# Kernel tuning notes

Hardware: AMD Instinct MI355X
Metric: run time of the kernel (lower is better)

## Reference

```python
import math
from collections import deque
import jax, jax.numpy as jnp
import numpy as np

PS = 16; DF = 256; DS = 16; DLANG = 896; BETA = 2.0
B_SZ = 2; IMG = 512


def setup_inputs():
    key = jax.random.key(0)
    ks = jax.random.split(key, 16)
    def rn(k, shape, scale=1.0):
        return jax.random.normal(k, shape, jnp.float32) * scale
    # W_delta bias init: inverse-softplus of dt ~ LogUniform(1e-3, 1e-1), as in torch _init_weights
    u = jax.random.uniform(ks[15], (DF,), jnp.float32)
    dt = jnp.exp(u * (math.log(0.1) - math.log(0.001)) + math.log(0.001))
    inv_dt = dt + jnp.log(-jnp.expm1(-dt))
    return {
        "images": rn(ks[0], (B_SZ, 3, IMG, IMG)),
        "lang_g": rn(ks[1], (B_SZ, DLANG)),
        "conv1_w": rn(ks[2], (64, 3, 3, 3), 1.0 / math.sqrt(27)),
        "conv1_b": jnp.zeros((64,), jnp.float32),
        "conv2_w": rn(ks[3], (128, 64, 3, 3), 1.0 / math.sqrt(576)),
        "conv2_b": jnp.zeros((128,), jnp.float32),
        "fc_w": rn(ks[4], (DF, 128), 1.0 / math.sqrt(128)),
        "fc_b": jnp.zeros((DF,), jnp.float32),
        "W_gate": rn(ks[5], (DF, DLANG), 1.0 / math.sqrt(DLANG)),
        "W_g_prime": rn(ks[6], (DF, DLANG), 1.0 / math.sqrt(DLANG)),
        "A_log": jnp.log(jnp.broadcast_to(jnp.arange(1, DS + 1, dtype=jnp.float32), (DF, DS))),
        "D": jnp.ones((DF,), jnp.float32),
        "B_w": rn(ks[7], (DS, DF), 1.0 / math.sqrt(DF)),
        "B_b": jnp.zeros((DS,), jnp.float32),
        "C_w": rn(ks[8], (DS, DF), 1.0 / math.sqrt(DF)),
        "C_b": jnp.zeros((DS,), jnp.float32),
        "Wd_w": rn(ks[9], (DF, DF), 1.0 / math.sqrt(DF)),
        "Wd_b": inv_dt,
        "out_w": rn(ks[10], (DF, DF), 1.0 / math.sqrt(DF)),
        "out_b": jnp.zeros((DF,), jnp.float32),
        "ln_g": jnp.ones((DF,), jnp.float32),
        "ln_b": jnp.zeros((DF,), jnp.float32),
    }


def _gelu(x):
    return jax.nn.gelu(x, approximate=False)  # torch nn.GELU() default = exact erf


def _conv(x, w, b):
    y = jax.lax.conv_general_dilated(x, w, (1, 1), 'SAME', dimension_numbers=('NCHW', 'OIHW', 'NCHW'))
    return y + b[None, :, None, None]


def _patch_feats(images, c1w, c1b, c2w, c2b, fcw, fcb):
    B, C, H, W = images.shape
    nH, nW = H // PS, W // PS
    # non-overlapping patchify (== unfold/unfold in torch)
    p = images.reshape(B, C, nH, PS, nW, PS).transpose(0, 2, 4, 1, 3, 5).reshape(B * nH * nW, C, PS, PS)
    h = _gelu(_conv(p, c1w, c1b))
    h = _gelu(_conv(h, c2w, c2b))
    h = h.mean(axis=(2, 3))  # AdaptiveAvgPool2d((1,1))
    feats = (h @ fcw.T + fcb).reshape(B, nH * nW, DF)
    return feats, nH, nW


def _structure(feats, r_sem, nH, nW):
    # Host-side (numpy) Kruskal MST + BFS ordering, mirroring the torch detach().cpu() path.
    f = np.asarray(feats, np.float32)
    r = np.asarray(r_sem, np.float32)
    B, P, _ = f.shape
    src, dst = [], []
    for i in range(nH):
        for j in range(nW):
            u = i * nW + j
            if j + 1 < nW:
                src.append(u); dst.append(u + 1)
            if i + 1 < nH:
                src.append(u); dst.append(u + nW)
    src = np.array(src); dst = np.array(dst)
    bfs_all, par_all = [], []
    for b in range(B):
        fn = f[b] / np.maximum(np.linalg.norm(f[b], axis=1, keepdims=True), 1e-12)
        cos = (fn[src] * fn[dst]).sum(1)
        w = (1.0 - r[b][src]) * (1.0 - r[b][dst]) * (-cos) + 1e-6
        parent = np.arange(P)
        def find(x):
            while parent[x] != x:
                parent[x] = parent[parent[x]]
                x = parent[x]
            return x
        adj = [[] for _ in range(P)]
        cnt = 0
        for idx in np.argsort(w):
            ru, rv = find(int(src[idx])), find(int(dst[idx]))
            if ru != rv:
                parent[ru] = rv
                adj[src[idx]].append(int(dst[idx]))
                adj[dst[idx]].append(int(src[idx]))
                cnt += 1
                if cnt == P - 1:
                    break
        root = int(r[b].argmax())
        vis = [False] * P; par_of = [-1] * P; bfs = []
        q = deque([root]); vis[root] = True
        while q:
            n = q.popleft()
            bfs.append(n)
            for nb in adj[n]:
                if not vis[nb]:
                    vis[nb] = True
                    par_of[nb] = n
                    q.append(nb)
        o2b = [0] * P
        for bi, oi in enumerate(bfs):
            o2b[oi] = bi
        par_bfs = [-1 if par_of[o] == -1 else o2b[par_of[o]] for o in bfs]
        bfs_all.append(bfs); par_all.append(par_bfs)
    return jnp.array(bfs_all, jnp.int32), jnp.array(par_all, jnp.int32)


def _core(feats, r_sem, g_prime, bfs, par, A_log, D, B_w, B_b, C_w, C_b, Wd_w, Wd_b, out_w, out_b, ln_g, ln_b):
    A = -jnp.exp(A_log)  # (DF, DS)
    def one(f_b, r_b, gp, bfs_b, par_b):
        rs = r_b[bfs_b]                                  # (P,)
        X = f_b[bfs_b] + rs[:, None] * gp[None, :]       # (P, DF)
        delta = jax.nn.softplus(X @ Wd_w.T + Wd_b) * (1.0 + BETA * rs[:, None])
        Bp = X @ B_w.T + B_b                             # (P, DS)
        Cp = X @ C_w.T + C_b                             # (P, DS)
        P = X.shape[0]
        def body(H, inp):
            i, d_i, b_i, c_i, x_i, p_i = inp
            A_bar = jnp.exp(d_i[:, None] * A)            # (DF, DS)
            h_par = H[jnp.maximum(p_i, 0)] * (p_i >= 0)  # zeros at root
            h = A_bar * h_par + (d_i[:, None] * b_i[None, :]) * x_i[:, None]
            H = H.at[i].set(h)
            y = (h * c_i[None, :]).sum(-1) + D * x_i
            return H, y
        H0 = jnp.zeros((P, DF, DS), X.dtype)
        _, Y = jax.lax.scan(body, H0, (jnp.arange(P), delta, Bp, Cp, X, par_b))
        Yr = jnp.zeros_like(Y).at[bfs_b].set(Y)          # scatter back to raster order
        o = Yr @ out_w.T + out_b
        mu = o.mean(-1, keepdims=True)
        v = ((o - mu) ** 2).mean(-1, keepdims=True)
        return ln_g * (o - mu) / jnp.sqrt(v + 1e-5) + ln_b
    return jax.vmap(one)(feats, r_sem, g_prime, bfs, par)


def reference(images, lang_g, conv1_w, conv1_b, conv2_w, conv2_b, fc_w, fc_b, W_gate, W_g_prime, A_log, D, B_w, B_b, C_w, C_b, Wd_w, Wd_b, out_w, out_b, ln_g, ln_b):
    feats, nH, nW = _patch_feats(images, conv1_w, conv1_b, conv2_w, conv2_b, fc_w, fc_b)
    g_proj = lang_g @ W_gate.T
    r_sem = jax.nn.sigmoid(jnp.einsum('bd,bpd->bp', g_proj, feats) / math.sqrt(DF))
    bfs, par = _structure(feats, r_sem, nH, nW)
    g_prime = lang_g @ W_g_prime.T
    return _core(feats, r_sem, g_prime, bfs, par, A_log, D, B_w, B_b, C_w, C_b, Wd_w, Wd_b, out_w, out_b, ln_g, ln_b)
```

## Files before the change

kernel.cpp:

```cpp
#include <hip/hip_runtime.h>
#include <cstddef>
#include <cstdint>

#define NB    2
#define NP    1024
#define DFEAT 256
#define DSTATE 16
#define NEDGE 1984

typedef unsigned short ushortb;

typedef float fx16 __attribute__((ext_vector_type(16)));
typedef short s16x8 __attribute__((ext_vector_type(8)));

__device__ __forceinline__ float bf2f(unsigned short u){
  union { unsigned int i; float f; } c; c.i = ((unsigned int)u) << 16; return c.f;
}
__device__ __forceinline__ unsigned short f2bf(float f){
  union { float f; unsigned int i; } c; c.f = f;
  unsigned int u = c.i;
  unsigned int r = (u + 0x7fffu + ((u >> 16) & 1u)) >> 16;
  return (unsigned short)r;
}
__device__ __forceinline__ float ldin(const void* p, size_t i, int isbf){
  return isbf ? bf2f(((const ushortb*)p)[i]) : ((const float*)p)[i];
}
__device__ __forceinline__ float gelu_f(float x){
  return 0.5f * x * (1.0f + erff(x * 0.70710678118654752f));
}
__device__ __forceinline__ unsigned int f2sort(float f){
  union { float f; unsigned int i; } c; c.f = f;
  return (c.i & 0x80000000u) ? ~c.i : (c.i | 0x80000000u);
}

constexpr size_t AL(size_t x){ return (x + 63) & ~(size_t)63; }
constexpr size_t O_W1    = 0;
constexpr size_t O_B1    = AL(O_W1 + 1728);
constexpr size_t O_W2    = AL(O_B1 + 64);
constexpr size_t O_B2    = AL(O_W2 + 73728);
constexpr size_t O_FCW   = AL(O_B2 + 128);
constexpr size_t O_FCB   = AL(O_FCW + 32768);
constexpr size_t O_WDW   = AL(O_FCB + 256);
constexpr size_t O_WDB   = AL(O_WDW + 65536);
constexpr size_t O_BWO   = AL(O_WDB + 256);
constexpr size_t O_BBO   = AL(O_BWO + 4096);
constexpr size_t O_CWO   = AL(O_BBO + 16);
constexpr size_t O_CBO   = AL(O_CWO + 4096);
constexpr size_t O_OW    = AL(O_CBO + 16);
constexpr size_t O_OB    = AL(O_OW + 65536);
constexpr size_t O_AF    = AL(O_OB + 256);
constexpr size_t O_DD    = AL(O_AF + 4096);
constexpr size_t O_LNG   = AL(O_DD + 256);
constexpr size_t O_LNB   = AL(O_LNG + 256);
constexpr size_t O_FEATS = AL(O_LNB + 256);
constexpr size_t O_GPROJ = AL(O_FEATS + (size_t)NB*NP*DFEAT);
constexpr size_t O_GPRIM = AL(O_GPROJ + NB*DFEAT);
constexpr size_t O_RSEM  = AL(O_GPRIM + NB*DFEAT);
constexpr size_t O_BFS   = AL(O_RSEM + NB*NP);
constexpr size_t O_PAR   = AL(O_BFS + NB*NP);
constexpr size_t O_X     = AL(O_PAR + NB*NP);
constexpr size_t O_DELTA = AL(O_X + (size_t)NB*NP*DFEAT);
constexpr size_t O_BP    = AL(O_DELTA + (size_t)NB*NP*DFEAT);
constexpr size_t O_CP    = AL(O_BP + NB*NP*DSTATE);
constexpr size_t O_YR    = AL(O_CP + NB*NP*DSTATE);
constexpr size_t O_FLAG  = AL(O_YR + (size_t)NB*NP*DFEAT);
constexpr size_t O_LVL   = AL(O_FLAG + 64);

__global__ __launch_bounds__(256) void k_sniff(const void* img, float* ws)
{
  __shared__ int cnt;
  int tid = threadIdx.x;
  if (tid == 0) cnt = 0;
  __syncthreads();
  const ushortb* u = (const ushortb*)img;
  int local = 0;
  for (int k = 0; k < 16; k++){
    unsigned short v = u[tid * 16 + k];
    if (v == 0 || v == 0x8000u){ local++; continue; }
    float f = fabsf(bf2f(v));
    if (f >= 1e-8f && f <= 64.f) local++;
  }
  atomicAdd(&cnt, local);
  __syncthreads();
  if (tid == 0) ((int*)(ws + O_FLAG))[0] = (cnt >= 3900) ? 1 : 0;
}

__global__ __launch_bounds__(256) void k_convert(const void* c1w, const void* c1b, const void* c2w,
                          const void* c2b, const void* fcw, const void* fcb,
                          const void* alog, const void* dvec,
                          const void* bw, const void* bb, const void* cw, const void* cb,
                          const void* wdw, const void* wdb,
                          const void* ow, const void* ob,
                          const void* lng, const void* lnb,
                          const void* lang, const void* wgate, const void* wgp,
                          float* ws)
{
  const int F = ((const int*)(ws + O_FLAG))[0];
  if (blockIdx.x >= 3038){
    int row = (blockIdx.x - 3038) * 4 + (threadIdx.x >> 6);
    int lane = threadIdx.x & 63;
    int mat = row >> 9;
    int b   = (row >> 8) & 1;
    int df  = row & 255;
    const void* W = mat ? wgp : wgate;
    float s = 0.f;
    for (int k = lane; k < 896; k += 64)
      s += ldin(lang, (size_t)b * 896 + k, F) * ldin(W, (size_t)df * 896 + k, F);
    s += __shfl_xor(s, 1);  s += __shfl_xor(s, 2);  s += __shfl_xor(s, 4);
    s += __shfl_xor(s, 8);  s += __shfl_xor(s, 16); s += __shfl_xor(s, 32);
    if (lane == 0) ws[(mat ? O_GPRIM : O_GPROJ) + b * 256 + df] = s;
    return;
  }
  if (blockIdx.x >= 990){
    size_t i2 = (size_t)(blockIdx.x - 990) * 256 + threadIdx.x;
    if (i2 < (size_t)NB * NP * DFEAT) ws[O_YR + i2] = 0.f;
    return;
  }
  int i = blockIdx.x * 256 + threadIdx.x;
  if (i < 1728){ ws[O_W1 + i] = ldin(c1w, i, F); return; } i -= 1728;
  if (i < 64){ ws[O_B1 + i] = ldin(c1b, i, F); return; } i -= 64;
  if (i < 73728){
    int sg = i >> 11;
    int r = i & 2047;
    int nt = r >> 9;
    int r2 = r & 511;
    int ln = r2 >> 3, e = r2 & 7;
    int c  = sg / 18, s = sg - c * 18;
    int tap = s >> 1, ksub = s & 1;
    int oc = nt * 32 + (ln & 31);
    int ic = c * 32 + ksub * 16 + (ln >> 5) * 8 + e;
    float v = ldin(c2w, (size_t)(oc * 64 + ic) * 9 + tap, F);
    ushortb hi = f2bf(v);
    float lo = v - bf2f(hi);
    ushortb* WB = (ushortb*)(ws + O_W2);
    size_t cb = ((size_t)(sg * 4 + nt)) * 2;
    WB[cb * 512 + r2]       = hi;
    WB[(cb + 1) * 512 + r2] = f2bf(lo);
    return;
  } i -= 73728;
  if (i < 128){ ws[O_B2 + i] = ldin(c2b, i, F); return; } i -= 128;
  if (i < 32768){ ws[O_FCW + i] = ldin(fcw, i, F); return; } i -= 32768;
  if (i < 256){ ws[O_FCB + i] = ldin(fcb, i, F); return; } i -= 256;
  if (i < 65536){
    int k = i >> 8, df = i & 255;
    ws[O_WDW + i] = ldin(wdw, (size_t)df * 256 + k, F); return;
  } i -= 65536;
  if (i < 256){ ws[O_WDB + i] = ldin(wdb, i, F); return; } i -= 256;
  if (i < 4096){
    int k = i >> 4, s = i & 15;
    ws[O_BWO + i] = ldin(bw, (size_t)s * 256 + k, F); return;
  } i -= 4096;
  if (i < 16){ ws[O_BBO + i] = ldin(bb, i, F); return; } i -= 16;
  if (i < 4096){
    int k = i >> 4, s = i & 15;
    ws[O_CWO + i] = ldin(cw, (size_t)s * 256 + k, F); return;
  } i -= 4096;
  if (i < 16){ ws[O_CBO + i] = ldin(cb, i, F); return; } i -= 16;
  if (i < 65536){
    int k = i >> 8, df = i & 255;
    ws[O_OW + i] = ldin(ow, (size_t)df * 256 + k, F); return;
  } i -= 65536;
  if (i < 256){ ws[O_OB + i] = ldin(ob, i, F); return; } i -= 256;
  if (i < 4096){ ws[O_AF + i] = -expf(ldin(alog, i, F)); return; } i -= 4096;
  if (i < 256){ ws[O_DD + i] = ldin(dvec, i, F); return; } i -= 256;
  if (i < 256){ ws[O_LNG + i] = ldin(lng, i, F); return; } i -= 256;
  if (i < 256){ ws[O_LNB + i] = ldin(lnb, i, F); }
}

__global__ __launch_bounds__(512, 4) void k_patch(const void* __restrict__ img,
                                                  const float* __restrict__ ws,
                                                  float* __restrict__ feats)
{
  __shared__ __align__(16) ushortb Abuf[2 * 11520];
  __shared__ float timg[768];
  __shared__ float pool8[512];
  __shared__ float pm[128];
  const int F = ((const int*)(ws + O_FLAG))[0];
  const float* W1 = ws + O_W1;  const float* B1 = ws + O_B1;
  const float* FCW = ws + O_FCW; const float* FCB = ws + O_FCB;
  const s16x8* BF = (const s16x8*)(ws + O_W2);

  int blk = blockIdx.x; int b = blk >> 10; int pidx = blk & 1023;
  int ph = pidx >> 5, pw = pidx & 31;
  int tid = threadIdx.x;
  uint4 z4 = make_uint4(0u, 0u, 0u, 0u);

  if (tid < 256){
    int y = tid >> 4, x = tid & 15;
    #pragma unroll
    for (int c = 0; c < 3; c++)
      timg[c * 256 + tid] =
        ldin(img, (((size_t)b * 3 + c) * 512 + (ph * 16 + y)) * 512 + (pw * 16 + x), F);
  }
  for (int z = tid; z < 320; z += 512){
    int plane = z / 160; int z2 = z - plane * 160;
    int cell = z2 >> 3, q = z2 & 7;
    int lr = cell >> 1; int gc = (cell & 1) ? 17 : 0;
    *(uint4*)&Abuf[plane * 11520 + ((lr * 18 + gc) << 6) + (q << 3)] = z4;
  }
  __syncthreads();

  int wv = tid >> 6, ln = tid & 63;
  int l31 = ln & 31, lhi = ln >> 5;
  int xcol = ln & 15, yrow = l31 >> 4;
  int mt = wv >> 1, ng = wv & 1;

  float psum0 = 0.f, psum1 = 0.f;

  for (int h = 0; h < 2; h++){
    {
      int pr = h ? 9 : 0;
      for (int z = tid; z < 256; z += 512){
        int plane = z >> 7; int z2 = z & 127;
        int gc = 1 + (z2 >> 3); int q = z2 & 7;
        *(uint4*)&Abuf[plane * 11520 + ((pr * 18 + gc) << 6) + (q << 3)] = z4;
      }
    }
    for (int u = tid; u < 1152; u += 512){
      int og = u / 144; int px = u - og * 144;
      int r9 = px >> 4, col = px & 15;
      int ir = h ? (7 + r9) : r9;
      float pin[27];
      #pragma unroll
      for (int cc = 0; cc < 3; cc++)
        #pragma unroll
        for (int dy = 0; dy < 3; dy++)
          #pragma unroll
          for (int dx = 0; dx < 3; dx++){
            int y = ir + dy - 1, x = col + dx - 1;
            bool ok = (y >= 0 && y < 16 && x >= 0 && x < 16);
            pin[cc * 9 + dy * 3 + dx] = ok ? timg[cc * 256 + y * 16 + x] : 0.f;
          }
      int oc0 = og * 8;
      float av[8];
      #pragma unroll
      for (int o = 0; o < 8; o++){
        float a = B1[oc0 + o];
        #pragma unroll
        for (int t = 0; t < 27; t++) a += W1[(oc0 + o) * 27 + t] * pin[t];
        av[o] = gelu_f(a);
      }
      unsigned int hp[4], lp[4];
      #pragma unroll
      for (int q = 0; q < 4; q++){
        float v0 = av[2 * q], v1 = av[2 * q + 1];
        ushortb h0 = f2bf(v0), h1 = f2bf(v1);
        float l0 = v0 - bf2f(h0), l1 = v1 - bf2f(h1);
        hp[q] = (unsigned int)h0 | ((unsigned int)h1 << 16);
        lp[q] = (unsigned int)f2bf(l0) | ((unsigned int)f2bf(l1) << 16);
      }
      int lr = h ? r9 : (r9 + 1);
      int gc = col + 1;
      int idx = ((lr * 18 + gc) << 6) + ((og ^ (gc & 7)) << 3);
      *(uint4*)&Abuf[idx] = make_uint4(hp[0], hp[1], hp[2], hp[3]);
      *(uint4*)&Abuf[11520 + idx] = make_uint4(lp[0], lp[1], lp[2], lp[3]);
    }
    __syncthreads();

    fx16 acc0, acc1;
    #pragma unroll
    for (int r = 0; r < 16; r++){ acc0[r] = 0.f; acc1[r] = 0.f; }
    {
      const s16x8* bq = BF + (size_t)((ng * 2) * 2) * 64 + ln;
      for (int sg = 0; sg < 36; sg++){
        int c = (sg >= 18) ? 1 : 0;
        int rem = sg - c * 18;
        int tap = rem >> 1, ksub = rem & 1;
        int dyq = tap / 3, dxq = tap - dyq * 3;
        int lr = 2 * mt + yrow + dyq;
        int gc = xcol + dxq;
        int slot = ((c * 2 + ksub) << 1) + lhi;
        int iA = ((lr * 18 + gc) << 6) + ((slot ^ (gc & 7)) << 3);
        s16x8 fa_h = *(const s16x8*)&Abuf[iA];
        s16x8 fa_l = *(const s16x8*)&Abuf[11520 + iA];
        s16x8 fb0h = bq[0];
        s16x8 fb0l = bq[64];
        s16x8 fb1h = bq[128];
        s16x8 fb1l = bq[192];
        acc0 = __builtin_amdgcn_mfma_f32_32x32x16_bf16(fa_h, fb0h, acc0, 0, 0, 0);
        acc1 = __builtin_amdgcn_mfma_f32_32x32x16_bf16(fa_h, fb1h, acc1, 0, 0, 0);
        acc0 = __builtin_amdgcn_mfma_f32_32x32x16_bf16(fa_l, fb0h, acc0, 0, 0, 0);
        acc1 = __builtin_amdgcn_mfma_f32_32x32x16_bf16(fa_l, fb1h, acc1, 0, 0, 0);
        acc0 = __builtin_amdgcn_mfma_f32_32x32x16_bf16(fa_h, fb0l, acc0, 0, 0, 0);
        acc1 = __builtin_amdgcn_mfma_f32_32x32x16_bf16(fa_h, fb1l, acc1, 0, 0, 0);
        bq += 512;
      }
    }
    {
      float bz0 = ws[O_B2 + (ng * 2) * 32 + l31];
      float bz1 = ws[O_B2 + (ng * 2 + 1) * 32 + l31];
      float s0 = 0.f, s1 = 0.f;
      #pragma unroll
      for (int r = 0; r < 16; r++){
        s0 += gelu_f(acc0[r] + bz0);
        s1 += gelu_f(acc1[r] + bz1);
      }
      psum0 += s0; psum1 += s1;
    }
    __syncthreads();
  }

  {
    float s0 = psum0 + __shfl_xor(psum0, 32);
    float s1 = psum1 + __shfl_xor(psum1, 32);
    if (lhi == 0){
      pool8[wv * 64 + l31] = s0;
      pool8[wv * 64 + 32 + l31] = s1;
    }
  }
  __syncthreads();
  if (tid < 128){
    int oc = tid; int nt = oc >> 5; int ngo = nt >> 1; int n = nt & 1; int l = oc & 31;
    float sv = pool8[(0 * 2 + ngo) * 64 + n * 32 + l]
             + pool8[(1 * 2 + ngo) * 64 + n * 32 + l]
             + pool8[(2 * 2 + ngo) * 64 + n * 32 + l]
             + pool8[(3 * 2 + ngo) * 64 + n * 32 + l];
    pm[oc] = sv * (1.f / 256.f);
  }
  __syncthreads();

  if (tid < 256){
    int df = tid;
    float s = FCB[df];
    const float* wrow = FCW + (size_t)df * 128;
    #pragma unroll
    for (int k = 0; k < 128; k += 4)
      s += wrow[k] * pm[k] + wrow[k + 1] * pm[k + 1]
         + wrow[k + 2] * pm[k + 2] + wrow[k + 3] * pm[k + 3];
    feats[((size_t)(b * 1024 + pidx)) * 256 + df] = s;
  }
}

__device__ __forceinline__ void edge_uv(int e, int& u, int& v){
  if (e < 1953){
    int i = e / 63; int k = e - i * 63;
    if (k < 62){ int j = k >> 1; u = i * 32 + j; v = (k & 1) ? u + 32 : u + 1; }
    else { u = i * 32 + 31; v = u + 32; }
  } else { u = 31 * 32 + (e - 1953); v = u + 1; }
}

__global__ __launch_bounds__(1024) void k_sx(float* __restrict__ ws)
{
  __shared__ float s_ninv[1024];
  __shared__ float s_w[NEDGE];
  __shared__ float s_r[1024];
  __shared__ int   s_comp[1024];
  __shared__ int   s_link[1024];
  __shared__ int   s_link2[1024];
  __shared__ unsigned long long s_best[1024];
  __shared__ unsigned char  s_mst[NEDGE];
  __shared__ unsigned short s_adj[1024 * 4];
  __shared__ unsigned char  s_deg[1024];
  __shared__ unsigned short s_bfs[1024];
  __shared__ short          s_parof[1024];
  __shared__ unsigned short s_o2b[1024];
  __shared__ unsigned short s_cur[1024];
  __shared__ unsigned short s_nxt[1024];
  __shared__ unsigned short s_off[1025];
  __shared__ unsigned short s_loff2[1026];
  __shared__ unsigned long long s_rootkey;
  __shared__ int s_ncomp, s_cursz, s_bfscnt, s_nextsz, s_nlvl;

  int tid = threadIdx.x;

  if (blockIdx.x >= 2){
    int gi = (int)(blockIdx.x - 2) * 4 + (tid >> 8);
    int b2 = gi >> 10, node = gi & 1023;
    int df = tid & 255;
    int wg = tid >> 8;
    float f = ws[O_FEATS + ((size_t)(b2 * 1024 + node)) * 256 + df];
    float v = f * ws[O_GPROJ + b2 * 256 + df];
    v += __shfl_xor(v, 1);  v += __shfl_xor(v, 2);  v += __shfl_xor(v, 4);
    v += __shfl_xor(v, 8);  v += __shfl_xor(v, 16); v += __shfl_xor(v, 32);
    if ((tid & 63) == 0) s_w[tid >> 6] = v;
    __syncthreads();
    float gdot = s_w[wg * 4] + s_w[wg * 4 + 1] + s_w[wg * 4 + 2] + s_w[wg * 4 + 3];
    float rs = 1.f / (1.f + expf(-gdot * (1.f / 16.f)));
    float xv = f + rs * ws[O_GPRIM + b2 * 256 + df];
    s_ninv[tid] = xv;
    ws[O_X + (size_t)gi * 256 + df] = xv;
    __syncthreads();
    {
      const float* WT = ws + O_WDW;
      const float* xg = s_ninv + wg * 256;
      float z = ws[O_WDB + df];
      #pragma unroll 8
      for (int k = 0; k < 256; k++)
        z += WT[(size_t)k * 256 + df] * xg[k];
      float sp = fmaxf(z, 0.f) + log1pf(expf(-fabsf(z)));
      ws[O_DELTA + (size_t)gi * 256 + df] = sp * (1.f + 2.f * rs);
    }
    if (df < 32){
      int s2 = df & 15;
      const float* WT = ws + ((df < 16) ? O_BWO : O_CWO);
      const float* xg = s_ninv + wg * 256;
      float a = ws[((df < 16) ? O_BBO : O_CBO) + s2];
      #pragma unroll 8
      for (int k = 0; k < 256; k++) a += WT[k * 16 + s2] * xg[k];
      ws[((df < 16) ? O_BP : O_CP) + (size_t)gi * 16 + s2] = a;
    }
    return;
  }

  int b = blockIdx.x;
  const float* feats = ws + O_FEATS + (size_t)b * NP * DFEAT;

  {
    const float4* f4 = (const float4*)(feats + (size_t)tid * 256);
    const float4* g4 = (const float4*)(ws + O_GPROJ + b * 256);
    float d = 0.f, gdot = 0.f;
    for (int k = 0; k < 64; k++){
      float4 q = f4[k]; float4 g = g4[k];
      d += q.x*q.x + q.y*q.y + q.z*q.z + q.w*q.w;
      gdot += q.x*g.x + q.y*g.y + q.z*g.z + q.w*g.w;
    }
    s_ninv[tid] = 1.f / fmaxf(sqrtf(d), 1e-12f);
    float r = 1.f / (1.f + expf(-gdot * (1.f / 16.f)));
    s_r[tid] = r;
    ws[O_RSEM + b * NP + tid] = r;
    s_comp[tid] = tid;
    s_deg[tid] = 0;
    s_bfs[tid] = (unsigned short)tid;
    s_o2b[tid] = (unsigned short)tid;
    s_parof[tid] = -1;
  }
  for (int e = tid; e < NEDGE; e += 1024) s_mst[e] = 0;
  __syncthreads();

  for (int e = tid; e < NEDGE; e += 1024){
    int u, v; edge_uv(e, u, v);
    const float4* fu = (const float4*)(feats + (size_t)u * 256);
    const float4* fv = (const float4*)(feats + (size_t)v * 256);
    float d = 0.f;
    for (int k = 0; k < 64; k++){ float4 a = fu[k], c = fv[k]; d += a.x*c.x + a.y*c.y + a.z*c.z + a.w*c.w; }
    float cosv = d * s_ninv[u] * s_ninv[v];
    s_w[e] = (1.f - s_r[u]) * (1.f - s_r[v]) * (-cosv) + 1e-6f;
  }
  __syncthreads();

  for (int round = 0; round < 12; round++){
    s_best[tid] = ~0ull;
    __syncthreads();
    for (int e = tid; e < NEDGE; e += 1024){
      int u, v; edge_uv(e, u, v);
      int cu = s_comp[u], cv = s_comp[v];
      if (cu != cv){
        unsigned long long key = (((unsigned long long)f2sort(s_w[e])) << 32) | (unsigned int)e;
        atomicMin(&s_best[cu], key);
        atomicMin(&s_best[cv], key);
      }
    }
    __syncthreads();
    int l = tid;
    if (s_comp[tid] == tid && s_best[tid] != ~0ull){
      int e = (int)(s_best[tid] & 0xffffffffu);
      int u, v; edge_uv(e, u, v);
      s_mst[e] = 1;
      int cu = s_comp[u], cv = s_comp[v];
      l = (cu == tid) ? cv : cu;
    }
    s_link[tid] = l;
    __syncthreads();
    if (l != tid && s_link[l] == tid && tid < l) s_link[tid] = tid;
    __syncthreads();
    {
      int x = tid;
      int p = s_link[x];
      while (p != x){ x = p; p = s_link[x]; }
      s_link2[tid] = x;
    }
    __syncthreads();
    s_comp[tid] = s_link2[s_comp[tid]];
    if (tid == 0) s_ncomp = 0;
    __syncthreads();
    if (s_comp[tid] == tid) atomicAdd(&s_ncomp, 1);
    __syncthreads();
    if (s_ncomp == 1) break;
    __syncthreads();
  }
  __syncthreads();

  {
    int v = tid; int i = v >> 5, j = v & 31;
    float wloc[4]; int nloc[4]; int d = 0;
    if (j > 0){ int e = (i < 31) ? (i * 63 + 2 * (j - 1)) : (1953 + (j - 1));
      if (s_mst[e]){ wloc[d] = s_w[e]; nloc[d] = v - 1; d++; } }
    if (j < 31){ int e = (i < 31) ? (i * 63 + 2 * j) : (1953 + j);
      if (s_mst[e]){ wloc[d] = s_w[e]; nloc[d] = v + 1; d++; } }
    if (i > 0){ int e = (i - 1) * 63 + ((j < 31) ? (2 * j + 1) : 62);
      if (s_mst[e]){ wloc[d] = s_w[e]; nloc[d] = v - 32; d++; } }
    if (i < 31){ int e = i * 63 + ((j < 31) ? (2 * j + 1) : 62);
      if (s_mst[e]){ wloc[d] = s_w[e]; nloc[d] = v + 32; d++; } }
    for (int a = 1; a < d; a++){
      float wv = wloc[a]; int nv = nloc[a]; int c = a - 1;
      while (c >= 0 && wloc[c] > wv){ wloc[c+1] = wloc[c]; nloc[c+1] = nloc[c]; c--; }
      wloc[c+1] = wv; nloc[c+1] = nv;
    }
    s_deg[v] = (unsigned char)d;
    for (int a = 0; a < d; a++) s_adj[v * 4 + a] = (unsigned short)nloc[a];
  }
  if (tid == 0) s_rootkey = 0ull;
  __syncthreads();
  {
    unsigned long long key = (((unsigned long long)f2sort(s_r[tid])) << 32) | (unsigned int)(1023 - tid);
    atomicMax(&s_rootkey, key);
  }
  __syncthreads();
  int root = 1023 - (int)(s_rootkey & 0xffffffffu);

  if (tid == 0){
    s_bfs[0] = (unsigned short)root; s_o2b[root] = 0; s_parof[root] = -1;
    s_cur[0] = (unsigned short)root; s_cursz = 1; s_bfscnt = 1; s_nlvl = 0;
  }
  __syncthreads();
  for (int lev = 0; lev < 1024; lev++){
    int csz = s_cursz;
    if (csz <= 0) break;
    if (tid < 64){
      int runbase = 0;
      for (int t0 = 0; t0 < csz; t0 += 64){
        int t = t0 + tid;
        int cnt = 0;
        if (t < csz){
          int n = s_cur[t];
          cnt = (int)s_deg[n] - (s_parof[n] >= 0 ? 1 : 0);
        }
        int v = cnt;
        #pragma unroll
        for (int off = 1; off < 64; off <<= 1){
          int u2 = __shfl_up(v, off);
          if (tid >= off) v += u2;
        }
        if (t < csz) s_off[t] = (unsigned short)(runbase + v - cnt);
        runbase += __shfl(v, 63);
      }
      if (tid == 0){
        if (s_nlvl < 1025){ s_loff2[s_nlvl] = (unsigned short)(s_bfscnt - csz); }
        s_nlvl++;
        s_nextsz = runbase;
      }
    }
    __syncthreads();
    if (tid < csz){
      int n = s_cur[tid]; int base = s_off[tid]; int k = 0;
      int pn = s_parof[n]; int dg = s_deg[n];
      for (int a = 0; a < dg; a++){
        int c = s_adj[n * 4 + a];
        if (c == pn) continue;
        s_parof[c] = (short)n;
        if (base + k < 1024) s_nxt[base + k] = (unsigned short)c;
        int pos = s_bfscnt + base + k;
        if (pos < 1024){
          s_bfs[pos] = (unsigned short)c;
          s_o2b[c] = (unsigned short)pos;
        }
        k++;
      }
    }
    __syncthreads();
    if (tid == 0){ s_bfscnt += s_nextsz; s_cursz = (s_nextsz > 1024) ? 1024 : s_nextsz; }
    __syncthreads();
    if (tid < s_cursz) s_cur[tid] = s_nxt[tid];
    __syncthreads();
  }
  __syncthreads();

  int* BFSo = (int*)(ws + O_BFS);
  int* PARo = (int*)(ws + O_PAR);
  {
    int node = s_bfs[tid] & 1023;
    BFSo[b * 1024 + tid] = node;
    int p = s_parof[node];
    PARo[b * 1024 + tid] = (p < 0) ? -1 : (int)(s_o2b[p] & 1023);
  }
  {
    int* LVLo = (int*)(ws + O_LVL) + b * 1040;
    int nl = s_nlvl; if (nl > 1024) nl = 1024;
    if (tid == 0){ LVLo[0] = nl; LVLo[1 + nl] = NP; }
    if (tid < nl) LVLo[1 + tid] = (int)s_loff2[tid];
  }
}

__global__ __launch_bounds__(256) void k_scan(float* __restrict__ ws)
{
  __shared__ float h[NP * DSTATE];
  __shared__ float xs[NP];
  __shared__ float ds[NP];
  __shared__ int   par_s[NP];
  __shared__ int   bfs_s[NP];
  int blk = blockIdx.x; int b = blk >> 8, f = blk & 255;
  int tid = threadIdx.x;
  int g = tid >> 4, s = tid & 15;
  const int* PARo = (const int*)(ws + O_PAR);
  const int* BFSo = (const int*)(ws + O_BFS);
  const int* LVLo = (const int*)(ws + O_LVL) + b * 1040;
  for (int i = tid; i < NP; i += 256){
    int node = BFSo[b * NP + i] & 1023;
    bfs_s[i] = node;
    par_s[i] = PARo[b * NP + i];
    xs[i] = ws[O_X     + ((size_t)(b * NP + node)) * DFEAT + f];
    ds[i] = ws[O_DELTA + ((size_t)(b * NP + node)) * DFEAT + f];
  }
  __syncthreads();

  int nlvl = LVLo[0];
  bool degen = (nlvl < 1 || nlvl > NP);
  if (degen) nlvl = NP;

  float Aln = ws[O_AF + f * 16 + s];
  float Dv  = ws[O_DD + f];
  const float* Bp = ws + O_BP + (size_t)b * NP * DSTATE;
  const float* Cp = ws + O_CP + (size_t)b * NP * DSTATE;
  float* Yr = ws + O_YR + (size_t)b * NP * DFEAT;

  for (int l = 0; l < nlvl; l++){
    int o0, o1;
    if (degen){ o0 = l; o1 = l + 1; }
    else {
      o0 = LVLo[1 + l]; o1 = LVLo[2 + l];
      o0 = (o0 < 0) ? 0 : ((o0 > NP) ? NP : o0);
      o1 = (o1 < o0) ? o0 : ((o1 > NP) ? NP : o1);
    }
    for (int i = o0 + g; i < o1; i += 16){
      int p = par_s[i];
      int node = bfs_s[i];
      float d = ds[i], x = xs[i];
      float hp = (p >= 0 && p < i) ? h[p * 16 + s] : 0.f;
      float hn = expf(d * Aln) * hp + d * Bp[node * 16 + s] * x;
      h[i * 16 + s] = hn;
      float t = hn * Cp[node * 16 + s];
      t += __shfl_xor(t, 1); t += __shfl_xor(t, 2);
      t += __shfl_xor(t, 4); t += __shfl_xor(t, 8);
      if (s == 0) Yr[(size_t)node * DFEAT + f] = t + Dv * x;
    }
    __syncthreads();
  }
}

__global__ __launch_bounds__(256) void k_outln(const float* __restrict__ ws,
                                               void* __restrict__ out)
{
  __shared__ float yl[256];
  __shared__ float red[8];
  const int F = ((const int*)(ws + O_FLAG))[0];
  int blk = blockIdx.x; int b = blk >> 10, p = blk & 1023; int df = threadIdx.x;
  yl[df] = ws[O_YR + ((size_t)(b * 1024 + p)) * 256 + df];
  __syncthreads();
  const float* OT = ws + O_OW;
  float a = ws[O_OB + df];
  #pragma unroll 8
  for (int k = 0; k < 256; k++)
    a += OT[(size_t)k * 256 + df] * yl[k];
  int lane = df & 63, wid = df >> 6;
  float t = a;
  t += __shfl_xor(t, 1); t += __shfl_xor(t, 2);  t += __shfl_xor(t, 4);
  t += __shfl_xor(t, 8); t += __shfl_xor(t, 16); t += __shfl_xor(t, 32);
  if (lane == 0) red[wid] = t;
  __syncthreads();
  float mu = (red[0] + red[1] + red[2] + red[3]) * (1.f / 256.f);
  float dv = a - mu;
  float t2 = dv * dv;
  t2 += __shfl_xor(t2, 1); t2 += __shfl_xor(t2, 2);  t2 += __shfl_xor(t2, 4);
  t2 += __shfl_xor(t2, 8); t2 += __shfl_xor(t2, 16); t2 += __shfl_xor(t2, 32);
  if (lane == 0) red[4 + wid] = t2;
  __syncthreads();
  float var = (red[4] + red[5] + red[6] + red[7]) * (1.f / 256.f);
  float o = ws[O_LNG + df] * dv / sqrtf(var + 1e-5f) + ws[O_LNB + df];
  size_t idx = ((size_t)(b * 1024 + p)) * 256 + df;
  if (F) ((ushortb*)out)[idx] = f2bf(o);
  else   ((float*)out)[idx]   = o;
}

extern "C" void kernel_launch(void* const* d_in, const int* in_sizes, int n_in,
                              void* d_out, int out_size, void* d_ws, size_t ws_size,
                              hipStream_t stream)
{
  (void)in_sizes; (void)n_in; (void)out_size; (void)ws_size;
  const void* img   = d_in[0];
  const void* lang  = d_in[1];
  const void* c1w   = d_in[2];
  const void* c1b   = d_in[3];
  const void* c2w   = d_in[4];
  const void* c2b   = d_in[5];
  const void* fcw   = d_in[6];
  const void* fcb   = d_in[7];
  const void* wgate = d_in[8];
  const void* wgp   = d_in[9];
  const void* alog  = d_in[10];
  const void* dvec  = d_in[11];
  const void* bw    = d_in[12];
  const void* bb    = d_in[13];
  const void* cw    = d_in[14];
  const void* cb    = d_in[15];
  const void* wdw   = d_in[16];
  const void* wdb   = d_in[17];
  const void* ow    = d_in[18];
  const void* ob    = d_in[19];
  const void* lng   = d_in[20];
  const void* lnb   = d_in[21];
  float* ws = (float*)d_ws;

  k_sniff<<<1, 256, 0, stream>>>(img, ws);
  k_convert<<<990 + 2048 + 256, 256, 0, stream>>>(c1w, c1b, c2w, c2b, fcw, fcb, alog, dvec,
                                                  bw, bb, cw, cb, wdw, wdb, ow, ob, lng, lnb,
                                                  lang, wgate, wgp, ws);
  k_patch<<<2048, 512, 0, stream>>>(img, ws, ws + O_FEATS);
  k_sx<<<2 + 512, 1024, 0, stream>>>(ws);
  k_scan<<<NB * DFEAT, 256, 0, stream>>>(ws);
  k_outln<<<2048, 256, 0, stream>>>(ws, d_out);
}
```

Baseline: 843.1 us.

## Batch multiple rows per block in projection and out-LN kernels, drop Yr zeroing

k_sx now computes two patch rows per 256-thread group, so each W_delta, B and C weight load feeds two accumulators. k_outln now handles four rows per block, sharing each out_w load across four dot products and running four LayerNorm reductions together. The zero-fill of the Yr buffer in k_convert is removed, on the assumption that the scan writes every node. The aim is to cut redundant weight traffic and block count, in exchange for more registers, lower parallelism, and reliance on the scan covering every Yr entry.

```diff
diff --git a/kernel.cpp b/kernel.cpp
--- a/kernel.cpp
+++ b/kernel.cpp
@@ -96,8 +96,8 @@
                           float* ws)
 {
   const int F = ((const int*)(ws + O_FLAG))[0];
-  if (blockIdx.x >= 3038){
-    int row = (blockIdx.x - 3038) * 4 + (threadIdx.x >> 6);
+  if (blockIdx.x >= 990){
+    int row = (blockIdx.x - 990) * 4 + (threadIdx.x >> 6);
     int lane = threadIdx.x & 63;
     int mat = row >> 9;
     int b   = (row >> 8) & 1;
@@ -109,11 +109,6 @@
     s += __shfl_xor(s, 1);  s += __shfl_xor(s, 2);  s += __shfl_xor(s, 4);
     s += __shfl_xor(s, 8);  s += __shfl_xor(s, 16); s += __shfl_xor(s, 32);
     if (lane == 0) ws[(mat ? O_GPRIM : O_GPROJ) + b * 256 + df] = s;
-    return;
-  }
-  if (blockIdx.x >= 990){
-    size_t i2 = (size_t)(blockIdx.x - 990) * 256 + threadIdx.x;
-    if (i2 < (size_t)NB * NP * DFEAT) ws[O_YR + i2] = 0.f;
     return;
   }
   int i = blockIdx.x * 256 + threadIdx.x;
@@ -364,40 +359,68 @@
   int tid = threadIdx.x;
 
   if (blockIdx.x >= 2){
-    int gi = (int)(blockIdx.x - 2) * 4 + (tid >> 8);
-    int b2 = gi >> 10, node = gi & 1023;
+    int wg = tid >> 8;
     int df = tid & 255;
-    int wg = tid >> 8;
-    float f = ws[O_FEATS + ((size_t)(b2 * 1024 + node)) * 256 + df];
-    float v = f * ws[O_GPROJ + b2 * 256 + df];
-    v += __shfl_xor(v, 1);  v += __shfl_xor(v, 2);  v += __shfl_xor(v, 4);
-    v += __shfl_xor(v, 8);  v += __shfl_xor(v, 16); v += __shfl_xor(v, 32);
-    if ((tid & 63) == 0) s_w[tid >> 6] = v;
-    __syncthreads();
-    float gdot = s_w[wg * 4] + s_w[wg * 4 + 1] + s_w[wg * 4 + 2] + s_w[wg * 4 + 3];
-    float rs = 1.f / (1.f + expf(-gdot * (1.f / 16.f)));
-    float xv = f + rs * ws[O_GPRIM + b2 * 256 + df];
-    s_ninv[tid] = xv;
-    ws[O_X + (size_t)gi * 256 + df] = xv;
+    int base = (int)(blockIdx.x - 2) * 8 + wg * 2;
+    int b2 = base >> 10;
+    int n0 = base & 1023, n1 = n0 + 1;
+    float f0 = ws[O_FEATS + ((size_t)(b2 * 1024 + n0)) * 256 + df];
+    float f1 = ws[O_FEATS + ((size_t)(b2 * 1024 + n1)) * 256 + df];
+    float gp = ws[O_GPROJ + b2 * 256 + df];
+    float v0 = f0 * gp, v1 = f1 * gp;
+    v0 += __shfl_xor(v0, 1);  v0 += __shfl_xor(v0, 2);  v0 += __shfl_xor(v0, 4);
+    v0 += __shfl_xor(v0, 8);  v0 += __shfl_xor(v0, 16); v0 += __shfl_xor(v0, 32);
+    v1 += __shfl_xor(v1, 1);  v1 += __shfl_xor(v1, 2);  v1 += __shfl_xor(v1, 4);
+    v1 += __shfl_xor(v1, 8);  v1 += __shfl_xor(v1, 16); v1 += __shfl_xor(v1, 32);
+    if ((tid & 63) == 0){
+      s_w[(tid >> 6) * 2]     = v0;
+      s_w[(tid >> 6) * 2 + 1] = v1;
+    }
+    __syncthreads();
+    float gd0 = s_w[(wg * 4 + 0) * 2] + s_w[(wg * 4 + 1) * 2]
+              + s_w[(wg * 4 + 2) * 2] + s_w[(wg * 4 + 3) * 2];
+    float gd1 = s_w[(wg * 4 + 0) * 2 + 1] + s_w[(wg * 4 + 1) * 2 + 1]
+              + s_w[(wg * 4 + 2) * 2 + 1] + s_w[(wg * 4 + 3) * 2 + 1];
+    float rs0 = 1.f / (1.f + expf(-gd0 * (1.f / 16.f)));
+    float rs1 = 1.f / (1.f + expf(-gd1 * (1.f / 16.f)));
+    float gpr = ws[O_GPRIM + b2 * 256 + df];
+    float xv0 = f0 + rs0 * gpr;
+    float xv1 = f1 + rs1 * gpr;
+    s_ninv[tid] = xv0;
+    s_r[tid]    = xv1;
+    ws[O_X + (size_t)(b2 * 1024 + n0) * 256 + df] = xv0;
+    ws[O_X + (size_t)(b2 * 1024 + n1) * 256 + df] = xv1;
     __syncthreads();
     {
       const float* WT = ws + O_WDW;
-      const float* xg = s_ninv + wg * 256;
-      float z = ws[O_WDB + df];
+      const float* xg0 = s_ninv + wg * 256;
+      const float* xg1 = s_r + wg * 256;
+      float z0 = ws[O_WDB + df], z1 = z0;
       #pragma unroll 8
-      for (int k = 0; k < 256; k++)
-        z += WT[(size_t)k * 256 + df] * xg[k];
-      float sp = fmaxf(z, 0.f) + log1pf(expf(-fabsf(z)));
-      ws[O_DELTA + (size_t)gi * 256 + df] = sp * (1.f + 2.f * rs);
+      for (int k = 0; k < 256; k++){
+        float w = WT[(size_t)k * 256 + df];
+        z0 += w * xg0[k];
+        z1 += w * xg1[k];
+      }
+      float sp0 = fmaxf(z0, 0.f) + log1pf(expf(-fabsf(z0)));
+      float sp1 = fmaxf(z1, 0.f) + log1pf(expf(-fabsf(z1)));
+      ws[O_DELTA + (size_t)(b2 * 1024 + n0) * 256 + df] = sp0 * (1.f + 2.f * rs0);
+      ws[O_DELTA + (size_t)(b2 * 1024 + n1) * 256 + df] = sp1 * (1.f + 2.f * rs1);
     }
     if (df < 32){
       int s2 = df & 15;
       const float* WT = ws + ((df < 16) ? O_BWO : O_CWO);
-      const float* xg = s_ninv + wg * 256;
-      float a = ws[((df < 16) ? O_BBO : O_CBO) + s2];
+      const float* xg0 = s_ninv + wg * 256;
+      const float* xg1 = s_r + wg * 256;
+      float a0 = ws[((df < 16) ? O_BBO : O_CBO) + s2], a1 = a0;
       #pragma unroll 8
-      for (int k = 0; k < 256; k++) a += WT[k * 16 + s2] * xg[k];
-      ws[((df < 16) ? O_BP : O_CP) + (size_t)gi * 16 + s2] = a;
+      for (int k = 0; k < 256; k++){
+        float w = WT[k * 16 + s2];
+        a0 += w * xg0[k];
+        a1 += w * xg1[k];
+      }
+      ws[((df < 16) ? O_BP : O_CP) + (size_t)(b2 * 1024 + n0) * 16 + s2] = a0;
+      ws[((df < 16) ? O_BP : O_CP) + (size_t)(b2 * 1024 + n1) * 16 + s2] = a1;
     }
     return;
   }
@@ -640,35 +663,76 @@
 __global__ __launch_bounds__(256) void k_outln(const float* __restrict__ ws,
                                                void* __restrict__ out)
 {
-  __shared__ float yl[256];
-  __shared__ float red[8];
+  __shared__ float yl[4][256];
+  __shared__ float red[4][8];
   const int F = ((const int*)(ws + O_FLAG))[0];
-  int blk = blockIdx.x; int b = blk >> 10, p = blk & 1023; int df = threadIdx.x;
-  yl[df] = ws[O_YR + ((size_t)(b * 1024 + p)) * 256 + df];
+  int blk = blockIdx.x;
+  int b = blk >> 8;
+  int p0 = (blk & 255) * 4;
+  int df = threadIdx.x;
+  #pragma unroll
+  for (int q = 0; q < 4; q++)
+    yl[q][df] = ws[O_YR + ((size_t)(b * 1024 + p0 + q)) * 256 + df];
   __syncthreads();
   const float* OT = ws + O_OW;
-  float a = ws[O_OB + df];
-  #pragma unroll 8
-  for (int k = 0; k < 256; k++)
-    a += OT[(size_t)k * 256 + df] * yl[k];
+  float ob0 = ws[O_OB + df];
+  float a0 = ob0, a1 = ob0, a2 = ob0, a3 = ob0;
+  #pragma unroll 4
+  for (int k = 0; k < 256; k++){
+    float ot = OT[(size_t)k * 256 + df];
+    a0 += ot * yl[0][k];
+    a1 += ot * yl[1][k];
+    a2 += ot * yl[2][k];
+    a3 += ot * yl[3][k];
+  }
   int lane = df & 63, wid = df >> 6;
-  float t = a;
-  t += __shfl_xor(t, 1); t += __shfl_xor(t, 2);  t += __shfl_xor(t, 4);
-  t += __shfl_xor(t, 8); t += __shfl_xor(t, 16); t += __shfl_xor(t, 32);
-  if (lane == 0) red[wid] = t;
-  __syncthreads();
-  float mu = (red[0] + red[1] + red[2] + red[3]) * (1.f / 256.f);
-  float dv = a - mu;
-  float t2 = dv * dv;
-  t2 += __shfl_xor(t2, 1); t2 += __shfl_xor(t2, 2);  t2 += __shfl_xor(t2, 4);
-  t2 += __shfl_xor(t2, 8); t2 += __shfl_xor(t2, 16); t2 += __shfl_xor(t2, 32);
-  if (lane == 0) red[4 + wid] = t2;
-  __syncthreads();
-  float var = (red[4] + red[5] + red[6] + red[7]) * (1.f / 256.f);
-  float o = ws[O_LNG + df] * dv / sqrtf(var + 1e-5f) + ws[O_LNB + df];
-  size_t idx = ((size_t)(b * 1024 + p)) * 256 + df;
-  if (F) ((ushortb*)out)[idx] = f2bf(o);
-  else   ((float*)out)[idx]   = o;
+  float aa0 = a0, aa1 = a1, aa2 = a2, aa3 = a3;
+  {
+    float t;
+    t = aa0; t += __shfl_xor(t,1); t += __shfl_xor(t,2); t += __shfl_xor(t,4);
+    t += __shfl_xor(t,8); t += __shfl_xor(t,16); t += __shfl_xor(t,32);
+    if (lane == 0) red[0][wid] = t;
+    t = aa1; t += __shfl_xor(t,1); t += __shfl_xor(t,2); t += __shfl_xor(t,4);
+    t += __shfl_xor(t,8); t += __shfl_xor(t,16); t += __shfl_xor(t,32);
+    if (lane == 0) red[1][wid] = t;
+    t = aa2; t += __shfl_xor(t,1); t += __shfl_xor(t,2); t += __shfl_xor(t,4);
+    t += __shfl_xor(t,8); t += __shfl_xor(t,16); t += __shfl_xor(t,32);
+    if (lane == 0) red[2][wid] = t;
+    t = aa3; t += __shfl_xor(t,1); t += __shfl_xor(t,2); t += __shfl_xor(t,4);
+    t += __shfl_xor(t,8); t += __shfl_xor(t,16); t += __shfl_xor(t,32);
+    if (lane == 0) red[3][wid] = t;
+  }
+  __syncthreads();
+  float dv0 = aa0 - (red[0][0] + red[0][1] + red[0][2] + red[0][3]) * (1.f / 256.f);
+  float dv1 = aa1 - (red[1][0] + red[1][1] + red[1][2] + red[1][3]) * (1.f / 256.f);
+  float dv2 = aa2 - (red[2][0] + red[2][1] + red[2][2] + red[2][3]) * (1.f / 256.f);
+  float dv3 = aa3 - (red[3][0] + red[3][1] + red[3][2] + red[3][3]) * (1.f / 256.f);
+  {
+    float t;
+    t = dv0 * dv0; t += __shfl_xor(t,1); t += __shfl_xor(t,2); t += __shfl_xor(t,4);
+    t += __shfl_xor(t,8); t += __shfl_xor(t,16); t += __shfl_xor(t,32);
+    if (lane == 0) red[0][4 + wid] = t;
+    t = dv1 * dv1; t += __shfl_xor(t,1); t += __shfl_xor(t,2); t += __shfl_xor(t,4);
+    t += __shfl_xor(t,8); t += __shfl_xor(t,16); t += __shfl_xor(t,32);
+    if (lane == 0) red[1][4 + wid] = t;
+    t = dv2 * dv2; t += __shfl_xor(t,1); t += __shfl_xor(t,2); t += __shfl_xor(t,4);
+    t += __shfl_xor(t,8); t += __shfl_xor(t,16); t += __shfl_xor(t,32);
+    if (lane == 0) red[2][4 + wid] = t;
+    t = dv3 * dv3; t += __shfl_xor(t,1); t += __shfl_xor(t,2); t += __shfl_xor(t,4);
+    t += __shfl_xor(t,8); t += __shfl_xor(t,16); t += __shfl_xor(t,32);
+    if (lane == 0) red[3][4 + wid] = t;
+  }
+  __syncthreads();
+  float lng = ws[O_LNG + df], lnb = ws[O_LNB + df];
+  #pragma unroll
+  for (int q = 0; q < 4; q++){
+    float dv = (q == 0) ? dv0 : (q == 1) ? dv1 : (q == 2) ? dv2 : dv3;
+    float var = (red[q][4] + red[q][5] + red[q][6] + red[q][7]) * (1.f / 256.f);
+    float o = lng * dv / sqrtf(var + 1e-5f) + lnb;
+    size_t idx = ((size_t)(b * 1024 + p0 + q)) * 256 + df;
+    if (F) ((ushortb*)out)[idx] = f2bf(o);
+    else   ((float*)out)[idx]   = o;
+  }
 }
 
 extern "C" void kernel_launch(void* const* d_in, const int* in_sizes, int n_in,
@@ -701,11 +765,11 @@
   float* ws = (float*)d_ws;
 
   k_sniff<<<1, 256, 0, stream>>>(img, ws);
-  k_convert<<<990 + 2048 + 256, 256, 0, stream>>>(c1w, c1b, c2w, c2b, fcw, fcb, alog, dvec,
-                                                  bw, bb, cw, cb, wdw, wdb, ow, ob, lng, lnb,
-                                                  lang, wgate, wgp, ws);
+  k_convert<<<990 + 256, 256, 0, stream>>>(c1w, c1b, c2w, c2b, fcw, fcb, alog, dvec,
+                                           bw, bb, cw, cb, wdw, wdb, ow, ob, lng, lnb,
+                                           lang, wgate, wgp, ws);
   k_patch<<<2048, 512, 0, stream>>>(img, ws, ws + O_FEATS);
-  k_sx<<<2 + 512, 1024, 0, stream>>>(ws);
+  k_sx<<<2 + 256, 1024, 0, stream>>>(ws);
   k_scan<<<NB * DFEAT, 256, 0, stream>>>(ws);
-  k_outln<<<2048, 256, 0, stream>>>(ws, d_out);
-}
+  k_outln<<<512, 256, 0, stream>>>(ws, d_out);
+}
```

Result: no change. 858.2 us (+1.8%).
